# Optimization experiments

Measured on AMD Instinct MI355X. Metric: run time of the kernel, lower is better.

The kernel has to match this reference:

```python
import jax, jax.numpy as jnp
import numpy as np

T, B, D, H = 512, 64, 1024, 1024  # seq_len, batch, input_dim, hidden (out_dim, bi_dir=False)


def setup_inputs() -> dict:
    key = jax.random.key(0)
    k = jax.random.split(key, 5)
    s = 1.0 / np.sqrt(H)  # PyTorch LSTMCell init scale
    x = jax.random.normal(k[0], (T, B, D), dtype=jnp.float32)
    W_ih = jax.random.uniform(k[1], (4 * H, D), minval=-s, maxval=s, dtype=jnp.float32)
    W_hh = jax.random.uniform(k[2], (4 * H, H), minval=-s, maxval=s, dtype=jnp.float32)
    b_ih = jax.random.uniform(k[3], (4 * H,), minval=-s, maxval=s, dtype=jnp.float32)
    b_hh = jax.random.uniform(k[4], (4 * H,), minval=-s, maxval=s, dtype=jnp.float32)
    return {"x": x, "W_ih": W_ih, "W_hh": W_hh, "b_ih": b_ih, "b_hh": b_hh}


def reference(x, W_ih, W_hh, b_ih, b_hh):
    # Unidirectional LSTM over [T, B, D] -> [T, B, H], PyTorch LSTMCell gate order i,f,g,o.
    # Precompute input contribution for all timesteps in one big GEMM.
    xg = jnp.einsum('tbd,gd->tbg', x, W_ih) + b_ih + b_hh  # [T, B, 4H]

    def step(carry, xg_t):
        h, c = carry
        gates = xg_t + h @ W_hh.T  # [B, 4H]
        i, f, g, o = jnp.split(gates, 4, axis=-1)
        c = jax.nn.sigmoid(f) * c + jax.nn.sigmoid(i) * jnp.tanh(g)
        h = jax.nn.sigmoid(o) * jnp.tanh(c)
        return (h, c), h

    h0 = jnp.zeros((B, H), dtype=x.dtype)
    c0 = jnp.zeros((B, H), dtype=x.dtype)
    _, hs = jax.lax.scan(step, (h0, c0), xg)  # hs: [T, B, H]
    return hs
```

## Files before the change

### kernel.cpp

```cpp
#include <hip/hip_runtime.h>
#include <hip/hip_bf16.h>
#include <stdint.h>

#define T_STEPS 512
#define BATCH   64
#define DIM     1024
#define HID     1024
#define NG      4096
#define MROWS   (T_STEPS * BATCH)

typedef __bf16 bf16;
typedef __bf16 bf16x4 __attribute__((ext_vector_type(4)));
typedef __bf16 bf16x8 __attribute__((ext_vector_type(8)));
typedef float  f32x4  __attribute__((ext_vector_type(4)));
typedef unsigned int u32;
typedef u32 u32x2 __attribute__((ext_vector_type(2)));
typedef u32 u32x4 __attribute__((ext_vector_type(4)));

__device__ __forceinline__ void g2lds16(const void* g, void* l) {
    __builtin_amdgcn_global_load_lds(
        (const __attribute__((address_space(1))) void*)g,
        (__attribute__((address_space(3))) void*)l, 16, 0, 0);
}

__device__ __forceinline__ float fsigmoid(float x) {
    return 1.0f / (1.0f + __expf(-x));
}
__device__ __forceinline__ float ftanh_(float x) {
    return 1.0f - 2.0f / (__expf(2.0f * x) + 1.0f);
}

__device__ __forceinline__ u32x4 load16_cc(const void* p) {
    u32x4 r;
    asm volatile("global_load_dwordx4 %0, %1, off sc0 sc1" : "=v"(r) : "v"(p) : "memory");
    return r;
}
__device__ __forceinline__ u32x2 load8_cached(const void* p) {
    u32x2 r;
    asm volatile("global_load_dwordx2 %0, %1, off" : "=v"(r) : "v"(p) : "memory");
    return r;
}
__device__ __forceinline__ void store2_cc(void* p, u32 v) {
    asm volatile("global_store_short %0, %1, off sc0 sc1" :: "v"(p), "v"(v) : "memory");
}
#define WAITVM(n) asm volatile("s_waitcnt vmcnt(" #n ")" ::: "memory")

__global__ __launch_bounds__(256) void prep_kernel(
    const float* __restrict__ x,   const float* __restrict__ wih,
    const float* __restrict__ whh, const float* __restrict__ bih,
    const float* __restrict__ bhh,
    bf16* __restrict__ xb, bf16* __restrict__ wihp, bf16* __restrict__ wfrag,
    float* __restrict__ bsump, bf16* __restrict__ hbuf, u32* __restrict__ flags)
{
    const int nt  = gridDim.x * blockDim.x;
    const int gid = blockIdx.x * blockDim.x + threadIdx.x;

    for (int i = gid; i < MROWS * DIM / 4; i += nt) {
        f32x4 v = *(const f32x4*)(x + (size_t)i * 4);
        bf16x4 o = {(bf16)v[0], (bf16)v[1], (bf16)v[2], (bf16)v[3]};
        *(bf16x4*)(xb + (size_t)i * 4) = o;
    }
    for (int i = gid; i < NG * (DIM / 4); i += nt) {
        const int n = i >> 8, c4 = (i & 255) * 4;
        f32x4 v = *(const f32x4*)(wih + (size_t)n * DIM + c4);
        bf16x4 o = {(bf16)v[0], (bf16)v[1], (bf16)v[2], (bf16)v[3]};
        const int np = ((n & 1023) << 2) | (n >> 10);
        *(bf16x4*)(wihp + (size_t)np * DIM + c4) = o;
    }
    for (int i = gid; i < NG * HID / 8; i += nt) {
        const int lane = i & 63;
        const int f    = (i >> 6) & 63;
        const int wv   = (i >> 12) & 3;
        const int hg   = i >> 14;
        const int n = f & 7, kk = f >> 3;
        const int grow = (lane & 3) * 1024 + hg * 32 + n * 4 + ((lane & 15) >> 2);
        const int k0   = wv * 256 + kk * 32 + (lane >> 4) * 8;
        f32x4 v0 = *(const f32x4*)(whh + (size_t)grow * HID + k0);
        f32x4 v1 = *(const f32x4*)(whh + (size_t)grow * HID + k0 + 4);
        bf16x8 o = {(bf16)v0[0], (bf16)v0[1], (bf16)v0[2], (bf16)v0[3],
                    (bf16)v1[0], (bf16)v1[1], (bf16)v1[2], (bf16)v1[3]};
        *(bf16x8*)(wfrag + (size_t)i * 8) = o;
    }
    for (int i = gid; i < NG; i += nt)
        bsump[((i & 1023) << 2) | (i >> 10)] = bih[i] + bhh[i];
    for (int i = gid; i < BATCH * HID / 4; i += nt) {
        bf16x4 z = {(bf16)0.f, (bf16)0.f, (bf16)0.f, (bf16)0.f};
        *(bf16x4*)(hbuf + (size_t)i * 4) = z;
    }
    for (int i = gid; i < 256 * 16; i += nt)
        flags[i] = 0u;
}

__global__ __launch_bounds__(256) void gemm_kernel(
    const bf16* __restrict__ A, const bf16* __restrict__ B,
    const float* __restrict__ bsum, bf16* __restrict__ xgp)
{
    __shared__ char lds[16384];
    char* As = lds;
    char* Bs = lds + 8192;

    const int tid  = threadIdx.x;
    const int lane = tid & 63;
    const int wv   = tid >> 6;
    const int wr   = wv >> 1, wc = wv & 1;
    const int bx   = blockIdx.x & 31;
    const int by   = blockIdx.x >> 5;
    const int m0   = by * 128, n0 = bx * 128;

    f32x4 acc[4][4] = {};

    const int r4 = tid >> 2;
    const int c8 = (tid & 3) * 8;
    const size_t arow0 = (size_t)(m0 +      r4) * DIM + c8;
    const size_t arow1 = (size_t)(m0 + 64 + r4) * DIM + c8;
    const size_t brow0 = (size_t)(n0 +      r4) * DIM + c8;
    const size_t brow1 = (size_t)(n0 + 64 + r4) * DIM + c8;
    const int ldsoff = tid * 16;

    for (int k0 = 0; k0 < DIM; k0 += 32) {
        g2lds16(A + arow0 + k0, As + ldsoff);
        g2lds16(A + arow1 + k0, As + 4096 + ldsoff);
        g2lds16(B + brow0 + k0, Bs + ldsoff);
        g2lds16(B + brow1 + k0, Bs + 4096 + ldsoff);
        __syncthreads();

        bf16x8 af[4], bfr[4];
        #pragma unroll
        for (int i = 0; i < 4; ++i) {
            af[i]  = *(const bf16x8*)(As + (wr*64 + i*16 + (lane & 15))*64 + (lane >> 4)*16);
            bfr[i] = *(const bf16x8*)(Bs + (wc*64 + i*16 + (lane & 15))*64 + (lane >> 4)*16);
        }
        #pragma unroll
        for (int i = 0; i < 4; ++i)
            #pragma unroll
            for (int j = 0; j < 4; ++j)
                acc[i][j] = __builtin_amdgcn_mfma_f32_16x16x32_bf16(
                    af[i], bfr[j], acc[i][j], 0, 0, 0);
        __syncthreads();
    }

    #pragma unroll
    for (int j = 0; j < 4; ++j) {
        const int nn = n0 + wc*64 + j*16 + (lane & 15);
        const float bias = bsum[nn];
        #pragma unroll
        for (int i = 0; i < 4; ++i) {
            #pragma unroll
            for (int r = 0; r < 4; ++r) {
                const int mm = m0 + wr*64 + i*16 + ((lane >> 4) << 2) + r;
                xgp[(size_t)mm * NG + nn] = (bf16)(acc[i][j][r] + bias);
            }
        }
    }
}

__global__ __launch_bounds__(256, 1) void lstm_kernel(
    const bf16* __restrict__ xgp, const bf16* __restrict__ wfrag,
    bf16* __restrict__ hbuf, u32* __restrict__ flags, float* __restrict__ out)
{
    __shared__ float gbuf[4][8][136];

    const int tid  = threadIdx.x;
    const int lane = tid & 63;
    const int wv   = tid >> 6;
    const int wg   = blockIdx.x;
    const int hg   = wg & 31;
    const int bg   = wg >> 5;

    bf16x8 wreg[64];
    {
        const bf16* wb = wfrag + ((size_t)(hg * 4 + wv) * 4096 + lane) * 8;
        #pragma unroll
        for (int f = 0; f < 64; ++f)
            wreg[f] = *(const bf16x8*)(wb + (size_t)f * 512);
    }

    const int frow  = lane & 15;
    const int hrow  = bg * 8 + (frow & 7);
    const int kbase = wv * 256 + (lane >> 4) * 8;
    const int b_el  = tid >> 5;
    const int j_el  = tid & 31;
    const int hid   = hg * 32 + j_el;

    const u32* pollp = flags + ((bg * 32 + wv * 8 + (lane & 7)) << 4);
    u32* myflag      = flags + ((bg * 32 + hg) << 4);

    float c = 0.f;
    u32x2 xr = load8_cached(xgp + (size_t)(bg * 8 + b_el) * NG + hid * 4);

    #pragma unroll 1
    for (int step = 0; step < T_STEPS; ++step) {
        while (__hip_atomic_load(pollp, __ATOMIC_RELAXED,
                                 __HIP_MEMORY_SCOPE_AGENT) < (u32)step)
            __builtin_amdgcn_s_sleep(1);

        const bf16* hb = hbuf + (step & 1) * (BATCH * HID) + (size_t)hrow * HID + kbase;
        u32x4 afr[8];
        #pragma unroll
        for (int kk = 0; kk < 8; ++kk)
            afr[kk] = load16_cc(hb + kk * 32);
        WAITVM(0);
        __builtin_amdgcn_sched_barrier(0);

        f32x4 acc[8] = {};
        #pragma unroll
        for (int kk = 0; kk < 8; ++kk) {
            bf16x8 a = __builtin_bit_cast(bf16x8, afr[kk]);
            #pragma unroll
            for (int n = 0; n < 8; ++n)
                acc[n] = __builtin_amdgcn_mfma_f32_16x16x32_bf16(
                    a, wreg[kk * 8 + n], acc[n], 0, 0, 0);
        }

        if (lane < 32) {
            const int q = lane >> 4;
            #pragma unroll
            for (int n = 0; n < 8; ++n)
                #pragma unroll
                for (int r = 0; r < 4; ++r)
                    gbuf[wv][q * 4 + r][n * 16 + frow] = acc[n][r];
        }
        __syncthreads();

        bf16x4 xv = __builtin_bit_cast(bf16x4, xr);
        float P[4];
        #pragma unroll
        for (int g = 0; g < 4; ++g)
            P[g] = gbuf[0][b_el][j_el * 4 + g] + gbuf[1][b_el][j_el * 4 + g]
                 + gbuf[2][b_el][j_el * 4 + g] + gbuf[3][b_el][j_el * 4 + g]
                 + (float)xv[g];
        const float ig = fsigmoid(P[0]);
        const float fg = fsigmoid(P[1]);
        const float gg = ftanh_(P[2]);
        const float og = fsigmoid(P[3]);
        c = fg * c + ig * gg;
        const float hv = og * ftanh_(c);

        const bf16 h16 = (bf16)hv;
        store2_cc(hbuf + ((step & 1) ^ 1) * (BATCH * HID)
                       + (size_t)(bg * 8 + b_el) * HID + hid,
                  (u32)__builtin_bit_cast(unsigned short, h16));
        WAITVM(0);
        __syncthreads();
        if (tid == 0)
            __hip_atomic_store(myflag, (u32)(step + 1),
                               __ATOMIC_RELAXED, __HIP_MEMORY_SCOPE_AGENT);

        out[(size_t)(step * BATCH + bg * 8 + b_el) * HID + hid] = hv;
        if (step + 1 < T_STEPS)
            xr = load8_cached(xgp + ((size_t)((step + 1) * BATCH) + bg * 8 + b_el) * NG
                                  + hid * 4);
    }
}

extern "C" void kernel_launch(void* const* d_in, const int* in_sizes, int n_in,
                              void* d_out, int out_size, void* d_ws, size_t ws_size,
                              hipStream_t stream) {
    const float* x   = (const float*)d_in[0];
    const float* wih = (const float*)d_in[1];
    const float* whh = (const float*)d_in[2];
    const float* bih = (const float*)d_in[3];
    const float* bhh = (const float*)d_in[4];
    float* out = (float*)d_out;

    char* ws = (char*)d_ws;
    size_t off = 0;
    bf16* xgp   = (bf16*)(ws + off); off += (size_t)MROWS * NG * 2;
    bf16* xb    = (bf16*)(ws + off); off += (size_t)MROWS * DIM * 2;
    bf16* wihp  = (bf16*)(ws + off); off += (size_t)NG * DIM * 2;
    bf16* wfrag = (bf16*)(ws + off); off += (size_t)NG * HID * 2;
    float* bsum = (float*)(ws + off); off += (size_t)NG * 4;
    bf16* hbuf  = (bf16*)(ws + off); off += (size_t)2 * BATCH * HID * 2;
    u32* flags  = (u32*)(ws + off); off += 256 * 16 * 4;
    (void)ws_size; (void)in_sizes; (void)n_in; (void)out_size;

    prep_kernel<<<2048, 256, 0, stream>>>(x, wih, whh, bih, bhh,
                                          xb, wihp, wfrag, bsum, hbuf, flags);
    gemm_kernel<<<8192, 256, 0, stream>>>(xb, wihp, bsum, xgp);
    lstm_kernel<<<256, 256, 0, stream>>>(xgp, wfrag, hbuf, flags, out);
}
```

Measured before the change: 2.213 ms.

## Replace flag-based step sync with step-tagged hidden-state words

Each hidden value is now stored as a 32-bit word that packs the bf16 value with the step number in the high half. Consumers poll the data itself, reloading until every tag matches the expected step. This removes the separate flag store, the store-wait and block barrier before publishing, and the extra flag round trip. The cost is twice the bytes per h load, repacking into bf16 fragments, and a double-buffered gbuf to avoid WAR hazards without the second syncthreads.

```diff
diff --git a/kernel.cpp b/kernel.cpp
--- a/kernel.cpp
+++ b/kernel.cpp
@@ -8,6 +8,7 @@
 #define HID     1024
 #define NG      4096
 #define MROWS   (T_STEPS * BATCH)
+#define HBUF_N  (BATCH * HID)
 
 typedef __bf16 bf16;
 typedef __bf16 bf16x4 __attribute__((ext_vector_type(4)));
@@ -40,8 +41,8 @@
     asm volatile("global_load_dwordx2 %0, %1, off" : "=v"(r) : "v"(p) : "memory");
     return r;
 }
-__device__ __forceinline__ void store2_cc(void* p, u32 v) {
-    asm volatile("global_store_short %0, %1, off sc0 sc1" :: "v"(p), "v"(v) : "memory");
+__device__ __forceinline__ void store4_cc(void* p, u32 v) {
+    asm volatile("global_store_dword %0, %1, off sc0 sc1" :: "v"(p), "v"(v) : "memory");
 }
 #define WAITVM(n) asm volatile("s_waitcnt vmcnt(" #n ")" ::: "memory")
 
@@ -50,7 +51,7 @@
     const float* __restrict__ whh, const float* __restrict__ bih,
     const float* __restrict__ bhh,
     bf16* __restrict__ xb, bf16* __restrict__ wihp, bf16* __restrict__ wfrag,
-    float* __restrict__ bsump, bf16* __restrict__ hbuf, u32* __restrict__ flags)
+    float* __restrict__ bsump, u32* __restrict__ hbuf32)
 {
     const int nt  = gridDim.x * blockDim.x;
     const int gid = blockIdx.x * blockDim.x + threadIdx.x;
@@ -83,12 +84,8 @@
     }
     for (int i = gid; i < NG; i += nt)
         bsump[((i & 1023) << 2) | (i >> 10)] = bih[i] + bhh[i];
-    for (int i = gid; i < BATCH * HID / 4; i += nt) {
-        bf16x4 z = {(bf16)0.f, (bf16)0.f, (bf16)0.f, (bf16)0.f};
-        *(bf16x4*)(hbuf + (size_t)i * 4) = z;
-    }
-    for (int i = gid; i < 256 * 16; i += nt)
-        flags[i] = 0u;
+    for (int i = gid; i < 2 * HBUF_N; i += nt)
+        hbuf32[i] = 0u;
 }
 
 __global__ __launch_bounds__(256) void gemm_kernel(
@@ -156,9 +153,9 @@
 
 __global__ __launch_bounds__(256, 1) void lstm_kernel(
     const bf16* __restrict__ xgp, const bf16* __restrict__ wfrag,
-    bf16* __restrict__ hbuf, u32* __restrict__ flags, float* __restrict__ out)
+    u32* __restrict__ hbuf32, float* __restrict__ out)
 {
-    __shared__ float gbuf[4][8][136];
+    __shared__ float gbuf[2][4][8][136];
 
     const int tid  = threadIdx.x;
     const int lane = tid & 63;
@@ -182,30 +179,44 @@
     const int j_el  = tid & 31;
     const int hid   = hg * 32 + j_el;
 
-    const u32* pollp = flags + ((bg * 32 + wv * 8 + (lane & 7)) << 4);
-    u32* myflag      = flags + ((bg * 32 + hg) << 4);
-
     float c = 0.f;
     u32x2 xr = load8_cached(xgp + (size_t)(bg * 8 + b_el) * NG + hid * 4);
 
     #pragma unroll 1
     for (int step = 0; step < T_STEPS; ++step) {
-        while (__hip_atomic_load(pollp, __ATOMIC_RELAXED,
-                                 __HIP_MEMORY_SCOPE_AGENT) < (u32)step)
+        const int pp = step & 1;
+        const u32* hb = hbuf32 + pp * HBUF_N + (size_t)hrow * HID + kbase;
+        const u32 exp_t = (u32)step << 16;
+
+        u32x4 raw[16];
+        for (;;) {
+            #pragma unroll
+            for (int kk = 0; kk < 8; ++kk) {
+                raw[2*kk]   = load16_cc(hb + kk * 32);
+                raw[2*kk+1] = load16_cc(hb + kk * 32 + 4);
+            }
+            WAITVM(0);
+            u32 bad = 0;
+            #pragma unroll
+            for (int i = 0; i < 16; ++i)
+                #pragma unroll
+                for (int j = 0; j < 4; ++j)
+                    bad |= raw[i][j] ^ exp_t;
+            if (__all((int)((bad >> 16) == 0))) break;
             __builtin_amdgcn_s_sleep(1);
-
-        const bf16* hb = hbuf + (step & 1) * (BATCH * HID) + (size_t)hrow * HID + kbase;
-        u32x4 afr[8];
-        #pragma unroll
-        for (int kk = 0; kk < 8; ++kk)
-            afr[kk] = load16_cc(hb + kk * 32);
-        WAITVM(0);
+        }
         __builtin_amdgcn_sched_barrier(0);
 
         f32x4 acc[8] = {};
         #pragma unroll
         for (int kk = 0; kk < 8; ++kk) {
-            bf16x8 a = __builtin_bit_cast(bf16x8, afr[kk]);
+            u32x4 lo = raw[2*kk], hi = raw[2*kk+1];
+            u32x4 pk;
+            pk[0] = (lo[0] & 0xFFFFu) | (lo[1] << 16);
+            pk[1] = (lo[2] & 0xFFFFu) | (lo[3] << 16);
+            pk[2] = (hi[0] & 0xFFFFu) | (hi[1] << 16);
+            pk[3] = (hi[2] & 0xFFFFu) | (hi[3] << 16);
+            bf16x8 a = __builtin_bit_cast(bf16x8, pk);
             #pragma unroll
             for (int n = 0; n < 8; ++n)
                 acc[n] = __builtin_amdgcn_mfma_f32_16x16x32_bf16(
@@ -218,7 +229,7 @@
             for (int n = 0; n < 8; ++n)
                 #pragma unroll
                 for (int r = 0; r < 4; ++r)
-                    gbuf[wv][q * 4 + r][n * 16 + frow] = acc[n][r];
+                    gbuf[pp][wv][q * 4 + r][n * 16 + frow] = acc[n][r];
         }
         __syncthreads();
 
@@ -226,8 +237,8 @@
         float P[4];
         #pragma unroll
         for (int g = 0; g < 4; ++g)
-            P[g] = gbuf[0][b_el][j_el * 4 + g] + gbuf[1][b_el][j_el * 4 + g]
-                 + gbuf[2][b_el][j_el * 4 + g] + gbuf[3][b_el][j_el * 4 + g]
+            P[g] = gbuf[pp][0][b_el][j_el * 4 + g] + gbuf[pp][1][b_el][j_el * 4 + g]
+                 + gbuf[pp][2][b_el][j_el * 4 + g] + gbuf[pp][3][b_el][j_el * 4 + g]
                  + (float)xv[g];
         const float ig = fsigmoid(P[0]);
         const float fg = fsigmoid(P[1]);
@@ -236,16 +247,10 @@
         c = fg * c + ig * gg;
         const float hv = og * ftanh_(c);
 
-        const bf16 h16 = (bf16)hv;
-        store2_cc(hbuf + ((step & 1) ^ 1) * (BATCH * HID)
-                       + (size_t)(bg * 8 + b_el) * HID + hid,
-                  (u32)__builtin_bit_cast(unsigned short, h16));
-        WAITVM(0);
-        __syncthreads();
-        if (tid == 0)
-            __hip_atomic_store(myflag, (u32)(step + 1),
-                               __ATOMIC_RELAXED, __HIP_MEMORY_SCOPE_AGENT);
-
+        const u32 hw = (u32)__builtin_bit_cast(unsigned short, (bf16)hv)
+                     | ((u32)(step + 1) << 16);
+        store4_cc(hbuf32 + ((step + 1) & 1) * HBUF_N
+                         + (size_t)(bg * 8 + b_el) * HID + hid, hw);
         out[(size_t)(step * BATCH + bg * 8 + b_el) * HID + hid] = hv;
         if (step + 1 < T_STEPS)
             xr = load8_cached(xgp + ((size_t)((step + 1) * BATCH) + bg * 8 + b_el) * NG
@@ -270,12 +275,11 @@
     bf16* wihp  = (bf16*)(ws + off); off += (size_t)NG * DIM * 2;
     bf16* wfrag = (bf16*)(ws + off); off += (size_t)NG * HID * 2;
     float* bsum = (float*)(ws + off); off += (size_t)NG * 4;
-    bf16* hbuf  = (bf16*)(ws + off); off += (size_t)2 * BATCH * HID * 2;
-    u32* flags  = (u32*)(ws + off); off += 256 * 16 * 4;
+    u32* hbuf32 = (u32*)(ws + off); off += (size_t)2 * HBUF_N * 4;
     (void)ws_size; (void)in_sizes; (void)n_in; (void)out_size;
 
     prep_kernel<<<2048, 256, 0, stream>>>(x, wih, whh, bih, bhh,
-                                          xb, wihp, wfrag, bsum, hbuf, flags);
+                                          xb, wihp, wfrag, bsum, hbuf32);
     gemm_kernel<<<8192, 256, 0, stream>>>(xb, wihp, bsum, xgp);
-    lstm_kernel<<<256, 256, 0, stream>>>(xgp, wfrag, hbuf, flags, out);
-}
+    lstm_kernel<<<256, 256, 0, stream>>>(xgp, wfrag, hbuf32, out);
+}
```

After: 2.805 ms. 26.7% more time.

## Replace per-block barrier flag with per-wave flags and speculative early poll

Applied to the files above, without the earlier changes.

Each wave now publishes its own per-step flag right after its h stores. This removes the trailing WAITVM(0) plus __syncthreads before a single block-level flag store. Consumers poll all four wave flags of each producer block, and the poll load is issued early, right after the h store, so the first check at the next step overlaps with the output and next-x loads. The gbuf LDS buffer is double-buffered by step parity, so dropping the second barrier stays safe. The risks are more flag traffic from four times as many flags, and subtle memory-ordering correctness, since each wave's flag only covers that wave's own stores.

```diff
diff --git a/kernel.cpp b/kernel.cpp
--- a/kernel.cpp
+++ b/kernel.cpp
@@ -35,13 +35,24 @@
     asm volatile("global_load_dwordx4 %0, %1, off sc0 sc1" : "=v"(r) : "v"(p) : "memory");
     return r;
 }
+__device__ __forceinline__ u32 ld4_cc(const u32* p) {
+    u32 r;
+    asm volatile("global_load_dword %0, %1, off sc0 sc1" : "=v"(r) : "v"(p) : "memory");
+    return r;
+}
+__device__ __forceinline__ void store2_cc(void* p, u32 v) {
+    asm volatile("global_store_short %0, %1, off sc0 sc1" :: "v"(p), "v"(v) : "memory");
+}
+__device__ __forceinline__ void st4_cc(u32* p, u32 v) {
+    asm volatile("global_store_dword %0, %1, off sc0 sc1" :: "v"(p), "v"(v) : "memory");
+}
 __device__ __forceinline__ u32x2 load8_cached(const void* p) {
     u32x2 r;
     asm volatile("global_load_dwordx2 %0, %1, off" : "=v"(r) : "v"(p) : "memory");
     return r;
 }
-__device__ __forceinline__ void store2_cc(void* p, u32 v) {
-    asm volatile("global_store_short %0, %1, off sc0 sc1" :: "v"(p), "v"(v) : "memory");
+__device__ __forceinline__ void store4_f32(float* p, float v) {
+    asm volatile("global_store_dword %0, %1, off" :: "v"(p), "v"(v) : "memory");
 }
 #define WAITVM(n) asm volatile("s_waitcnt vmcnt(" #n ")" ::: "memory")
 
@@ -87,7 +98,7 @@
         bf16x4 z = {(bf16)0.f, (bf16)0.f, (bf16)0.f, (bf16)0.f};
         *(bf16x4*)(hbuf + (size_t)i * 4) = z;
     }
-    for (int i = gid; i < 256 * 16; i += nt)
+    for (int i = gid; i < 256 * 4 * 16; i += nt)
         flags[i] = 0u;
 }
 
@@ -158,7 +169,7 @@
     const bf16* __restrict__ xgp, const bf16* __restrict__ wfrag,
     bf16* __restrict__ hbuf, u32* __restrict__ flags, float* __restrict__ out)
 {
-    __shared__ float gbuf[4][8][136];
+    __shared__ float gbuf[2][4][8][136];
 
     const int tid  = threadIdx.x;
     const int lane = tid & 63;
@@ -182,17 +193,27 @@
     const int j_el  = tid & 31;
     const int hid   = hg * 32 + j_el;
 
-    const u32* pollp = flags + ((bg * 32 + wv * 8 + (lane & 7)) << 4);
-    u32* myflag      = flags + ((bg * 32 + hg) << 4);
+    const u32* pollp = flags
+        + ((size_t)((bg * 32 + wv * 8 + (lane & 7)) * 4 + ((lane >> 3) & 3)) << 4);
+    u32* myflag = flags + ((size_t)((bg * 32 + hg) * 4 + wv) << 4);
 
     float c = 0.f;
+    u32 pollv = 0u;
     u32x2 xr = load8_cached(xgp + (size_t)(bg * 8 + b_el) * NG + hid * 4);
 
     #pragma unroll 1
     for (int step = 0; step < T_STEPS; ++step) {
-        while (__hip_atomic_load(pollp, __ATOMIC_RELAXED,
-                                 __HIP_MEMORY_SCOPE_AGENT) < (u32)step)
-            __builtin_amdgcn_s_sleep(1);
+        if (step > 0) {
+            WAITVM(3);
+            asm volatile("" : "+v"(pollv));
+            if (!__all((int)(pollv >= (u32)step))) {
+                do {
+                    __builtin_amdgcn_s_sleep(1);
+                    pollv = __hip_atomic_load(pollp, __ATOMIC_RELAXED,
+                                              __HIP_MEMORY_SCOPE_AGENT);
+                } while (!__all((int)(pollv >= (u32)step)));
+            }
+        }
 
         const bf16* hb = hbuf + (step & 1) * (BATCH * HID) + (size_t)hrow * HID + kbase;
         u32x4 afr[8];
@@ -212,13 +233,14 @@
                     a, wreg[kk * 8 + n], acc[n], 0, 0, 0);
         }
 
+        const int pp = step & 1;
         if (lane < 32) {
             const int q = lane >> 4;
             #pragma unroll
             for (int n = 0; n < 8; ++n)
                 #pragma unroll
                 for (int r = 0; r < 4; ++r)
-                    gbuf[wv][q * 4 + r][n * 16 + frow] = acc[n][r];
+                    gbuf[pp][wv][q * 4 + r][n * 16 + frow] = acc[n][r];
         }
         __syncthreads();
 
@@ -226,8 +248,8 @@
         float P[4];
         #pragma unroll
         for (int g = 0; g < 4; ++g)
-            P[g] = gbuf[0][b_el][j_el * 4 + g] + gbuf[1][b_el][j_el * 4 + g]
-                 + gbuf[2][b_el][j_el * 4 + g] + gbuf[3][b_el][j_el * 4 + g]
+            P[g] = gbuf[pp][0][b_el][j_el * 4 + g] + gbuf[pp][1][b_el][j_el * 4 + g]
+                 + gbuf[pp][2][b_el][j_el * 4 + g] + gbuf[pp][3][b_el][j_el * 4 + g]
                  + (float)xv[g];
         const float ig = fsigmoid(P[0]);
         const float fg = fsigmoid(P[1]);
@@ -240,13 +262,12 @@
         store2_cc(hbuf + ((step & 1) ^ 1) * (BATCH * HID)
                        + (size_t)(bg * 8 + b_el) * HID + hid,
                   (u32)__builtin_bit_cast(unsigned short, h16));
-        WAITVM(0);
-        __syncthreads();
-        if (tid == 0)
-            __hip_atomic_store(myflag, (u32)(step + 1),
-                               __ATOMIC_RELAXED, __HIP_MEMORY_SCOPE_AGENT);
-
-        out[(size_t)(step * BATCH + bg * 8 + b_el) * HID + hid] = hv;
+        pollv = ld4_cc(pollp);
+        WAITVM(1);
+        __builtin_amdgcn_sched_barrier(0);
+        if (lane == 0)
+            st4_cc(myflag, (u32)(step + 1));
+        store4_f32(out + (size_t)(step * BATCH + bg * 8 + b_el) * HID + hid, hv);
         if (step + 1 < T_STEPS)
             xr = load8_cached(xgp + ((size_t)((step + 1) * BATCH) + bg * 8 + b_el) * NG
                                   + hid * 4);
@@ -271,7 +292,7 @@
     bf16* wfrag = (bf16*)(ws + off); off += (size_t)NG * HID * 2;
     float* bsum = (float*)(ws + off); off += (size_t)NG * 4;
     bf16* hbuf  = (bf16*)(ws + off); off += (size_t)2 * BATCH * HID * 2;
-    u32* flags  = (u32*)(ws + off); off += 256 * 16 * 4;
+    u32* flags  = (u32*)(ws + off); off += 256 * 4 * 16 * 4;
     (void)ws_size; (void)in_sizes; (void)n_in; (void)out_size;
 
     prep_kernel<<<2048, 256, 0, stream>>>(x, wih, whh, bih, bhh,
```

Measured after the change: 2.411 ms. 8.9% more time.
